# Performance work log

Hardware: AMD Instinct MI355X
Metric: run time of the kernel (lower is better)

## Reference

```python
import jax, jax.numpy as jnp
import numpy as np

B, LQ, LK, D = 8, 2048, 2048, 1024


def setup_inputs() -> dict:
    key = jax.random.key(0)
    k1, k2, k3, k4, k5 = jax.random.split(key, 5)
    inp = jax.random.normal(k1, (B, LQ, D), dtype=jnp.float32)
    memory = jax.random.normal(k2, (B, LK, D), dtype=jnp.float32)
    # 0/1 float mask over memory positions (1 = masked out)
    mask = (jax.random.uniform(k3, (B, LK)) < 0.15).astype(jnp.float32)
    # nn.Linear(D, 1, bias=False): weight shape [1, D], kaiming-uniform-ish init
    w_input = jax.random.uniform(k4, (1, D), dtype=jnp.float32,
                                 minval=-1.0 / np.sqrt(D), maxval=1.0 / np.sqrt(D))
    # dot_scale ~ U(0, 1/sqrt(D)) per original .uniform_(1/input_size**0.5)
    dot_scale = jax.random.uniform(k5, (D,), dtype=jnp.float32,
                                   minval=0.0, maxval=1.0 / np.sqrt(D))
    return {"input": inp, "memory": memory, "mask": mask,
            "w_input": w_input, "dot_scale": dot_scale}


def reference(input, memory, mask, w_input, dot_scale):
    # input_dot: Linear(D,1,bias=False) -> [B, Lq, 1]
    input_dot = jnp.einsum('bqd,od->bqo', input, w_input)  # o == 1
    # cross_dot: (input * dot_scale) @ memory^T -> [B, Lq, Lk]
    cross_dot = jnp.einsum('bqd,bkd->bqk', input * dot_scale, memory)
    att = input_dot + cross_dot - 1e30 * mask[:, None, :]
    weight_one = jax.nn.softmax(att, axis=-1)  # [B, Lq, Lk]
    output_one = jnp.einsum('bqk,bkd->bqd', weight_one, memory)
    return output_one
```

## Files before the change

kernel.cpp:

```cpp
#include <hip/hip_runtime.h>

#define B_  8
#define LQ_ 2048
#define LK_ 2048
#define D_  1024

typedef unsigned short u16;
using short8  = __attribute__((ext_vector_type(8))) short;
using floatx4 = __attribute__((ext_vector_type(4))) float;

#define GAS __attribute__((address_space(1)))
#define LAS __attribute__((address_space(3)))

__device__ __forceinline__ u16 f2bf(float f) {
  unsigned u = __float_as_uint(f);
  u += 0x7fffu + ((u >> 16) & 1u);
  return (u16)(u >> 16);
}
__device__ __forceinline__ float bf2f(u16 h) {
  return __uint_as_float(((unsigned)h) << 16);
}

__global__ void prep_q(const float* __restrict__ in, const float* __restrict__ ds,
                       u16* __restrict__ qb) {
  const int n4 = B_ * LQ_ * D_ / 4;
  int stride = gridDim.x * blockDim.x;
  for (int i = blockIdx.x * blockDim.x + threadIdx.x; i < n4; i += stride) {
    float4 v = ((const float4*)in)[i];
    float4 s = ((const float4*)ds)[i & (D_ / 4 - 1)];
    ushort4 o;
    o.x = f2bf(v.x * s.x); o.y = f2bf(v.y * s.y);
    o.z = f2bf(v.z * s.z); o.w = f2bf(v.w * s.w);
    ((ushort4*)qb)[i] = o;
  }
}

__global__ void prep_m(const float* __restrict__ mem, u16* __restrict__ mb,
                       u16* __restrict__ mbT) {
  __shared__ u16 tile[32][33];
  int tx = threadIdx.x, ty = threadIdx.y;
  int k0 = blockIdx.x * 32, d0 = blockIdx.y * 32, b = blockIdx.z;
  const float* mB = mem + (size_t)b * LK_ * D_;
  u16* mbB = mb  + (size_t)b * LK_ * D_;
  u16* mtB = mbT + (size_t)b * D_ * LK_;
#pragma unroll
  for (int i = 0; i < 4; i++) {
    int r = ty + i * 8;
    float v = mB[(size_t)(k0 + r) * D_ + d0 + tx];
    u16 h = f2bf(v);
    mbB[(size_t)(k0 + r) * D_ + d0 + tx] = h;
    tile[r][tx] = h;
  }
  __syncthreads();
#pragma unroll
  for (int i = 0; i < 4; i++) {
    int r = ty + i * 8;
    mtB[(size_t)(d0 + r) * LK_ + k0 + tx] = tile[tx][r];
  }
}

template <bool OUT_BF16>
__global__ void gemm_bt(const u16* __restrict__ A, const u16* __restrict__ Bm,
                        void* __restrict__ C, int K, int lda, int ldb, int ldc,
                        size_t sA, size_t sB, size_t sC) {
  __shared__ __align__(16) u16 As[128 * 32];
  __shared__ __align__(16) u16 Bs[128 * 32];
  int tid = threadIdx.x;
  int lane = tid & 63, w = tid >> 6;
  int wm = (w >> 1) * 64, wn = (w & 1) * 64;
  int lm = lane & 15, quad = lane >> 4;
  int bz = blockIdx.z;

  const u16* Ab = A  + (size_t)bz * sA + (size_t)(blockIdx.y * 128) * lda;
  const u16* Bb = Bm + (size_t)bz * sB + (size_t)(blockIdx.x * 128) * ldb;

  int c0 = tid, c1 = tid + 256;
  const u16* gA0 = Ab + (size_t)(c0 >> 2) * lda + (c0 & 3) * 8;
  const u16* gA1 = Ab + (size_t)(c1 >> 2) * lda + (c1 & 3) * 8;
  const u16* gB0 = Bb + (size_t)(c0 >> 2) * ldb + (c0 & 3) * 8;
  const u16* gB1 = Bb + (size_t)(c1 >> 2) * ldb + (c1 & 3) * 8;
  u16* lA0 = As + c0 * 8; u16* lA1 = As + c1 * 8;
  u16* lB0 = Bs + c0 * 8; u16* lB1 = Bs + c1 * 8;

  floatx4 acc[4][4];
#pragma unroll
  for (int mi = 0; mi < 4; mi++)
#pragma unroll
    for (int ni = 0; ni < 4; ni++)
      acc[mi][ni] = {0.f, 0.f, 0.f, 0.f};

  for (int k0 = 0; k0 < K; k0 += 32) {
    __builtin_amdgcn_global_load_lds((GAS void*)(gA0 + k0), (LAS void*)lA0, 16, 0, 0);
    __builtin_amdgcn_global_load_lds((GAS void*)(gA1 + k0), (LAS void*)lA1, 16, 0, 0);
    __builtin_amdgcn_global_load_lds((GAS void*)(gB0 + k0), (LAS void*)lB0, 16, 0, 0);
    __builtin_amdgcn_global_load_lds((GAS void*)(gB1 + k0), (LAS void*)lB1, 16, 0, 0);
    __syncthreads();

    short8 af[4], bf[4];
#pragma unroll
    for (int mi = 0; mi < 4; mi++)
      af[mi] = *(const short8*)(As + ((wm + mi * 16 + lm) << 5) + (quad << 3));
#pragma unroll
    for (int ni = 0; ni < 4; ni++)
      bf[ni] = *(const short8*)(Bs + ((wn + ni * 16 + lm) << 5) + (quad << 3));
#pragma unroll
    for (int mi = 0; mi < 4; mi++)
#pragma unroll
      for (int ni = 0; ni < 4; ni++)
        acc[mi][ni] = __builtin_amdgcn_mfma_f32_16x16x32_bf16(af[mi], bf[ni],
                                                              acc[mi][ni], 0, 0, 0);
    __syncthreads();
  }

  int gm0 = blockIdx.y * 128 + wm + quad * 4;
  int gn0 = blockIdx.x * 128 + wn + lm;
  size_t cb = (size_t)bz * sC;
#pragma unroll
  for (int mi = 0; mi < 4; mi++) {
#pragma unroll
    for (int r = 0; r < 4; r++) {
      size_t rowoff = cb + (size_t)(gm0 + mi * 16 + r) * ldc + gn0;
#pragma unroll
      for (int ni = 0; ni < 4; ni++) {
        float v = acc[mi][ni][r];
        if constexpr (OUT_BF16)
          ((u16*)C)[rowoff + ni * 16] = f2bf(v);
        else
          ((float*)C)[rowoff + ni * 16] = v;
      }
    }
  }
}

__global__ void softmax_rows(u16* __restrict__ S, const float* __restrict__ mask) {
  int row = blockIdx.x;
  int b = row >> 11;
  u16* srow = S + (size_t)row * LK_;
  const float* mrow = mask + (size_t)b * LK_;
  int tid = threadIdx.x;
  int lane = tid & 63, wid = tid >> 6;

  float s[8]; bool mk[8];
  float lmax = -1e30f;
#pragma unroll
  for (int j = 0; j < 8; j++) {
    int k = tid + 256 * j;
    float v = bf2f(srow[k]);
    bool m = (mrow[k] != 0.0f);
    s[j] = v; mk[j] = m;
    if (!m) lmax = fmaxf(lmax, v);
  }
#pragma unroll
  for (int off = 32; off > 0; off >>= 1)
    lmax = fmaxf(lmax, __shfl_xor(lmax, off, 64));
  __shared__ float red[4];
  if (lane == 0) red[wid] = lmax;
  __syncthreads();
  float rmax = fmaxf(fmaxf(red[0], red[1]), fmaxf(red[2], red[3]));

  float lsum = 0.f;
#pragma unroll
  for (int j = 0; j < 8; j++) {
    float e = mk[j] ? 0.f : __expf(s[j] - rmax);
    s[j] = e; lsum += e;
  }
#pragma unroll
  for (int off = 32; off > 0; off >>= 1)
    lsum += __shfl_xor(lsum, off, 64);
  __syncthreads();
  if (lane == 0) red[wid] = lsum;
  __syncthreads();
  float inv = 1.f / (red[0] + red[1] + red[2] + red[3]);
#pragma unroll
  for (int j = 0; j < 8; j++) {
    int k = tid + 256 * j;
    srow[k] = f2bf(s[j] * inv);
  }
}

extern "C" void kernel_launch(void* const* d_in, const int* in_sizes, int n_in,
                              void* d_out, int out_size, void* d_ws, size_t ws_size,
                              hipStream_t stream) {
  const float* input  = (const float*)d_in[0];
  const float* memory = (const float*)d_in[1];
  const float* mask   = (const float*)d_in[2];
  const float* dscale = (const float*)d_in[4];

  char* ws = (char*)d_ws;
  u16* qb  = (u16*)(ws);
  u16* mb  = (u16*)(ws + (size_t)32 * 1024 * 1024);
  u16* mbT = (u16*)(ws + (size_t)64 * 1024 * 1024);
  u16* S   = (u16*)(ws + (size_t)96 * 1024 * 1024);
  float* out = (float*)d_out;

  hipLaunchKernelGGL(prep_q, dim3(2048), dim3(256), 0, stream, input, dscale, qb);
  hipLaunchKernelGGL(prep_m, dim3(LK_ / 32, D_ / 32, B_), dim3(32, 8), 0, stream,
                     memory, mb, mbT);
  hipLaunchKernelGGL((gemm_bt<true>), dim3(LK_ / 128, LQ_ / 128, B_), dim3(256), 0,
                     stream, qb, mb, (void*)S, D_, D_, D_, LK_,
                     (size_t)LQ_ * D_, (size_t)LK_ * D_, (size_t)LQ_ * LK_);
  hipLaunchKernelGGL(softmax_rows, dim3(B_ * LQ_), dim3(256), 0, stream, S, mask);
  hipLaunchKernelGGL((gemm_bt<false>), dim3(D_ / 128, LQ_ / 128, B_), dim3(256), 0,
                     stream, S, mbT, (void*)out, LK_, LK_, LK_, D_,
                     (size_t)LQ_ * LK_, (size_t)D_ * LK_, (size_t)LQ_ * D_);
}
```

Baseline: 391.0 us.

## Fuse mask into score GEMM epilogue, vectorize softmax and transpose, swizzle tiles

The score GEMM epilogue now writes bf16 -inf for masked columns, so softmax no longer reads the mask and can use 16-byte vector loads and stores per thread. The prep_m transpose moves to 64x64 tiles with float4 loads and ushort4 stores. GEMM blocks are remapped so the batch index varies fastest and M tiles are grouped by 8, aiming for better L2 reuse. One risk is a row where every key is masked: the max becomes -inf and the exponentials produce NaN, where the old code did not.

```diff
diff --git a/kernel.cpp b/kernel.cpp
--- a/kernel.cpp
+++ b/kernel.cpp
@@ -37,31 +37,39 @@
 
 __global__ void prep_m(const float* __restrict__ mem, u16* __restrict__ mb,
                        u16* __restrict__ mbT) {
-  __shared__ u16 tile[32][33];
-  int tx = threadIdx.x, ty = threadIdx.y;
-  int k0 = blockIdx.x * 32, d0 = blockIdx.y * 32, b = blockIdx.z;
+  __shared__ u16 tile[64][68];
+  int tid = threadIdx.x;
+  int tx = tid & 15, ty = tid >> 4;
+  int k0 = blockIdx.x * 64, d0 = blockIdx.y * 64, b = blockIdx.z;
   const float* mB = mem + (size_t)b * LK_ * D_;
   u16* mbB = mb  + (size_t)b * LK_ * D_;
   u16* mtB = mbT + (size_t)b * D_ * LK_;
 #pragma unroll
   for (int i = 0; i < 4; i++) {
-    int r = ty + i * 8;
-    float v = mB[(size_t)(k0 + r) * D_ + d0 + tx];
-    u16 h = f2bf(v);
-    mbB[(size_t)(k0 + r) * D_ + d0 + tx] = h;
-    tile[r][tx] = h;
+    int r = ty + 16 * i;
+    float4 v = *(const float4*)(mB + (size_t)(k0 + r) * D_ + d0 + tx * 4);
+    ushort4 h;
+    h.x = f2bf(v.x); h.y = f2bf(v.y); h.z = f2bf(v.z); h.w = f2bf(v.w);
+    *(ushort4*)(mbB + (size_t)(k0 + r) * D_ + d0 + tx * 4) = h;
+    *(ushort4*)(&tile[r][tx * 4]) = h;
   }
   __syncthreads();
 #pragma unroll
   for (int i = 0; i < 4; i++) {
-    int r = ty + i * 8;
-    mtB[(size_t)(d0 + r) * LK_ + k0 + tx] = tile[tx][r];
-  }
-}
-
-template <bool OUT_BF16>
+    int rr = ty + 16 * i;
+    ushort4 o;
+    o.x = tile[tx * 4 + 0][rr];
+    o.y = tile[tx * 4 + 1][rr];
+    o.z = tile[tx * 4 + 2][rr];
+    o.w = tile[tx * 4 + 3][rr];
+    *(ushort4*)(mtB + (size_t)(d0 + rr) * LK_ + k0 + tx * 4) = o;
+  }
+}
+
+template <int MODE>
 __global__ void gemm_bt(const u16* __restrict__ A, const u16* __restrict__ Bm,
-                        void* __restrict__ C, int K, int lda, int ldb, int ldc,
+                        void* __restrict__ C, const float* __restrict__ mask,
+                        int K, int lda, int ldb, int ldc,
                         size_t sA, size_t sB, size_t sC) {
   __shared__ __align__(16) u16 As[128 * 32];
   __shared__ __align__(16) u16 Bs[128 * 32];
@@ -69,10 +77,20 @@
   int lane = tid & 63, w = tid >> 6;
   int wm = (w >> 1) * 64, wn = (w & 1) * 64;
   int lm = lane & 15, quad = lane >> 4;
-  int bz = blockIdx.z;
-
-  const u16* Ab = A  + (size_t)bz * sA + (size_t)(blockIdx.y * 128) * lda;
-  const u16* Bb = Bm + (size_t)bz * sB + (size_t)(blockIdx.x * 128) * ldb;
+
+  int tiles_n = gridDim.x;
+  int bid = (blockIdx.z * gridDim.y + blockIdx.y) * tiles_n + blockIdx.x;
+  int bz = bid & 7;
+  int s = bid >> 3;
+  const int GM = 8;
+  int per_group = GM * tiles_n;
+  int group = s / per_group;
+  int rem = s - group * per_group;
+  int tm = group * GM + (rem & (GM - 1));
+  int tn = rem >> 3;
+
+  const u16* Ab = A  + (size_t)bz * sA + (size_t)(tm * 128) * lda;
+  const u16* Bb = Bm + (size_t)bz * sB + (size_t)(tn * 128) * ldb;
 
   int c0 = tid, c1 = tid + 256;
   const u16* gA0 = Ab + (size_t)(c0 >> 2) * lda + (c0 & 3) * 8;
@@ -112,9 +130,17 @@
     __syncthreads();
   }
 
-  int gm0 = blockIdx.y * 128 + wm + quad * 4;
-  int gn0 = blockIdx.x * 128 + wn + lm;
+  int gm0 = tm * 128 + wm + quad * 4;
+  int gn0 = tn * 128 + wn + lm;
   size_t cb = (size_t)bz * sC;
+
+  bool msk[4];
+  if constexpr (MODE == 1) {
+    const float* mrow = mask + (size_t)bz * LK_;
+#pragma unroll
+    for (int ni = 0; ni < 4; ni++) msk[ni] = (mrow[gn0 + ni * 16] != 0.0f);
+  }
+
 #pragma unroll
   for (int mi = 0; mi < 4; mi++) {
 #pragma unroll
@@ -123,8 +149,8 @@
 #pragma unroll
       for (int ni = 0; ni < 4; ni++) {
         float v = acc[mi][ni][r];
-        if constexpr (OUT_BF16)
-          ((u16*)C)[rowoff + ni * 16] = f2bf(v);
+        if constexpr (MODE == 1)
+          ((u16*)C)[rowoff + ni * 16] = msk[ni] ? (u16)0xFF80 : f2bf(v);
         else
           ((float*)C)[rowoff + ni * 16] = v;
       }
@@ -132,24 +158,22 @@
   }
 }
 
-__global__ void softmax_rows(u16* __restrict__ S, const float* __restrict__ mask) {
+__global__ void softmax_rows(u16* __restrict__ S) {
   int row = blockIdx.x;
-  int b = row >> 11;
   u16* srow = S + (size_t)row * LK_;
-  const float* mrow = mask + (size_t)b * LK_;
   int tid = threadIdx.x;
   int lane = tid & 63, wid = tid >> 6;
 
-  float s[8]; bool mk[8];
-  float lmax = -1e30f;
-#pragma unroll
-  for (int j = 0; j < 8; j++) {
-    int k = tid + 256 * j;
-    float v = bf2f(srow[k]);
-    bool m = (mrow[k] != 0.0f);
-    s[j] = v; mk[j] = m;
-    if (!m) lmax = fmaxf(lmax, v);
-  }
+  uint4 raw = *(const uint4*)(srow + tid * 8);
+  float s[8];
+  s[0] = bf2f((u16)(raw.x & 0xffff)); s[1] = bf2f((u16)(raw.x >> 16));
+  s[2] = bf2f((u16)(raw.y & 0xffff)); s[3] = bf2f((u16)(raw.y >> 16));
+  s[4] = bf2f((u16)(raw.z & 0xffff)); s[5] = bf2f((u16)(raw.z >> 16));
+  s[6] = bf2f((u16)(raw.w & 0xffff)); s[7] = bf2f((u16)(raw.w >> 16));
+
+  float lmax = s[0];
+#pragma unroll
+  for (int j = 1; j < 8; j++) lmax = fmaxf(lmax, s[j]);
 #pragma unroll
   for (int off = 32; off > 0; off >>= 1)
     lmax = fmaxf(lmax, __shfl_xor(lmax, off, 64));
@@ -161,7 +185,7 @@
   float lsum = 0.f;
 #pragma unroll
   for (int j = 0; j < 8; j++) {
-    float e = mk[j] ? 0.f : __expf(s[j] - rmax);
+    float e = __expf(s[j] - rmax);
     s[j] = e; lsum += e;
   }
 #pragma unroll
@@ -171,11 +195,13 @@
   if (lane == 0) red[wid] = lsum;
   __syncthreads();
   float inv = 1.f / (red[0] + red[1] + red[2] + red[3]);
-#pragma unroll
-  for (int j = 0; j < 8; j++) {
-    int k = tid + 256 * j;
-    srow[k] = f2bf(s[j] * inv);
-  }
+
+  uint4 out;
+  out.x = (unsigned)f2bf(s[0] * inv) | ((unsigned)f2bf(s[1] * inv) << 16);
+  out.y = (unsigned)f2bf(s[2] * inv) | ((unsigned)f2bf(s[3] * inv) << 16);
+  out.z = (unsigned)f2bf(s[4] * inv) | ((unsigned)f2bf(s[5] * inv) << 16);
+  out.w = (unsigned)f2bf(s[6] * inv) | ((unsigned)f2bf(s[7] * inv) << 16);
+  *(uint4*)(srow + tid * 8) = out;
 }
 
 extern "C" void kernel_launch(void* const* d_in, const int* in_sizes, int n_in,
@@ -194,13 +220,13 @@
   float* out = (float*)d_out;
 
   hipLaunchKernelGGL(prep_q, dim3(2048), dim3(256), 0, stream, input, dscale, qb);
-  hipLaunchKernelGGL(prep_m, dim3(LK_ / 32, D_ / 32, B_), dim3(32, 8), 0, stream,
+  hipLaunchKernelGGL(prep_m, dim3(LK_ / 64, D_ / 64, B_), dim3(256), 0, stream,
                      memory, mb, mbT);
-  hipLaunchKernelGGL((gemm_bt<true>), dim3(LK_ / 128, LQ_ / 128, B_), dim3(256), 0,
-                     stream, qb, mb, (void*)S, D_, D_, D_, LK_,
+  hipLaunchKernelGGL((gemm_bt<1>), dim3(LK_ / 128, LQ_ / 128, B_), dim3(256), 0,
+                     stream, qb, mb, (void*)S, mask, D_, D_, D_, LK_,
                      (size_t)LQ_ * D_, (size_t)LK_ * D_, (size_t)LQ_ * LK_);
-  hipLaunchKernelGGL(softmax_rows, dim3(B_ * LQ_), dim3(256), 0, stream, S, mask);
-  hipLaunchKernelGGL((gemm_bt<false>), dim3(D_ / 128, LQ_ / 128, B_), dim3(256), 0,
-                     stream, S, mbT, (void*)out, LK_, LK_, LK_, D_,
+  hipLaunchKernelGGL(softmax_rows, dim3(B_ * LQ_), dim3(256), 0, stream, S);
+  hipLaunchKernelGGL((gemm_bt<0>), dim3(D_ / 128, LQ_ / 128, B_), dim3(256), 0,
+                     stream, S, mbT, (void*)out, nullptr, LK_, LK_, LK_, D_,
                      (size_t)LQ_ * LK_, (size_t)D_ * LK_, (size_t)LQ_ * D_);
 }
```

Result: faster. 352.4 us (-9.9%).
